# Kernel optimization log

Hardware: AMD Instinct MI355X
Metric: run time of the kernel (lower is better)

Reference implementation:

```python
import jax, jax.numpy as jnp
import numpy as np

EPS = 1e-5
SLOPE = 0.2

def _leaky(x):
    return jnp.where(x >= 0, x, SLOPE * x)

def _bn(x, g, b, axes):
    # batch-norm in training mode: biased stats over `axes`, per remaining channel dim
    mu = jnp.mean(x, axis=axes, keepdims=True)
    var = jnp.var(x, axis=axes, keepdims=True)
    shape = [1] * x.ndim
    shape[2 if x.ndim == 5 else 1] = -1
    return (x - mu) * jax.lax.rsqrt(var + EPS) * g.reshape(shape) + b.reshape(shape)

def setup_inputs() -> dict:
    key = jax.random.key(0)
    ks = jax.random.split(key, 6)
    T, B, C, H, W, D = 17, 16, 512, 16, 16, 256
    return {
        "cond": jax.random.normal(ks[0], (B, D), jnp.float32),
        "xbar": jax.random.normal(ks[1], (T, B, C, H, W), jnp.float32),
        "lin_w": jax.random.normal(ks[2], (D, D), jnp.float32) * 0.05,
        "lin_b": jnp.zeros((D,), jnp.float32),
        "bn_s_g": jnp.ones((D,), jnp.float32),
        "bn_s_b": jnp.zeros((D,), jnp.float32),
        "conv1_w": jax.random.normal(ks[3], (C, C), jnp.float32) * 0.05,
        "bn1_g": jnp.ones((C,), jnp.float32),
        "bn1_b": jnp.zeros((C,), jnp.float32),
        "conv2_w": jax.random.normal(ks[4], (C, C + D), jnp.float32) * 0.05,
        "bn2_g": jnp.ones((C,), jnp.float32),
        "bn2_b": jnp.zeros((C,), jnp.float32),
        "conv3_w": jax.random.normal(ks[5], (1, C, 2, 2), jnp.float32) * 0.05,
    }

def reference(cond, xbar, lin_w, lin_b, bn_s_g, bn_s_b, conv1_w, bn1_g, bn1_b, conv2_w, bn2_g, bn2_b, conv3_w):
    # sent_map: Linear -> BatchNorm1d (over batch) -> LeakyReLU
    sent = cond @ lin_w.T + lin_b                       # [B, D]
    sent = _leaky(_bn(sent, bn_s_g, bn_s_b, axes=(0,)))

    motions = xbar[1:] - xbar[:-1]                      # [F, B, C, H, W]
    F, B, C, H, W = motions.shape

    # motion_map: 1x1 conv -> BN (per-frame stats, matching the python loop) -> LeakyReLU
    h = jnp.einsum('fbchw,oc->fbohw', motions, conv1_w)
    h = _leaky(_bn(h, bn1_g, bn1_b, axes=(1, 3, 4)))

    # broadcast sentence vector over space (replaces per-pixel python loop)
    sent_dupe = jnp.broadcast_to(sent[None, :, :, None, None], (F, B, sent.shape[1], H, W))
    ms = jnp.concatenate([h, sent_dupe], axis=2)        # [F, B, C+D, H, W]

    # predictor: 1x1 conv -> BN (per-frame) -> LeakyReLU -> 2x2 stride-2 conv
    h2 = jnp.einsum('fbchw,oc->fbohw', ms, conv2_w)
    h2 = _leaky(_bn(h2, bn2_g, bn2_b, axes=(1, 3, 4)))

    h2f = h2.reshape(F * B, C, H, W)
    out = jax.lax.conv_general_dilated(
        h2f, conv3_w, window_strides=(2, 2), padding='VALID',
        dimension_numbers=('NCHW', 'OIHW', 'NCHW'))     # [F*B, 1, H/2, W/2]
    return out.reshape(F, B, -1)                        # matches view(B,-1) per frame + stack
```

## Files before the change

### kernel.cpp

```cpp
#include <hip/hip_runtime.h>
#include <hip/hip_bf16.h>

#define EPS 1e-5f
#define SLOPE 0.2f

#define NF 16
#define NBATCH 16
#define NC 512
#define NHW 256
#define ND 256
#define K2 768
#define MF 4096
#define FRAME_ELEMS ((size_t)MF * NC)

typedef __attribute__((ext_vector_type(8))) short short8;
typedef __attribute__((ext_vector_type(4))) float float4v;

__device__ __forceinline__ float lrelu(float v) { return v >= 0.f ? v : SLOPE * v; }
__device__ __forceinline__ float b2f(ushort u) { union { float f; uint i; } x; x.i = ((uint)u) << 16; return x.f; }
__device__ __forceinline__ ushort f2b(float f) {
  uint i = __float_as_uint(f);
  return (ushort)((i + 0x7FFFu + ((i >> 16) & 1u)) >> 16);
}
__device__ __forceinline__ void gl16(const ushort* g, ushort* l) {
  __builtin_amdgcn_global_load_lds(
      (const __attribute__((address_space(1))) unsigned int*)g,
      (__attribute__((address_space(3))) unsigned int*)l, 16, 0, 0);
}

__global__ __launch_bounds__(256) void k_pre(
    const float* __restrict__ w1, const float* __restrict__ w2,
    const float* __restrict__ cond, const float* __restrict__ lin_w,
    const float* __restrict__ lin_b, const float* __restrict__ gam,
    const float* __restrict__ bet,
    ushort* __restrict__ w1b, ushort* __restrict__ w2b,
    float* __restrict__ sent) {
  int bx = blockIdx.x, t = threadIdx.x;
  if (bx < 1024) {
    int i = bx * 256 + t;
    w1b[i] = f2b(w1[i]);
    int o = i >> 9, c = i & 511;
    w2b[i] = f2b(w2[(size_t)o * K2 + c]);
    return;
  }
  int d = t;
  float acc[NBATCH];
  float bias = lin_b[d];
#pragma unroll
  for (int b = 0; b < NBATCH; ++b) acc[b] = bias;
  for (int k = 0; k < ND; ++k) {
    float w = lin_w[d * ND + k];
#pragma unroll
    for (int b = 0; b < NBATCH; ++b) acc[b] = fmaf(cond[b * ND + k], w, acc[b]);
  }
  float mu = 0.f;
#pragma unroll
  for (int b = 0; b < NBATCH; ++b) mu += acc[b];
  mu *= (1.f / NBATCH);
  float var = 0.f;
#pragma unroll
  for (int b = 0; b < NBATCH; ++b) { float x = acc[b] - mu; var = fmaf(x, x, var); }
  var *= (1.f / NBATCH);
  float sc = rsqrtf(var + EPS) * gam[d];
  float sh = bet[d] - mu * sc;
#pragma unroll
  for (int b = 0; b < NBATCH; ++b) sent[b * ND + d] = lrelu(fmaf(acc[b], sc, sh));
}

__global__ __launch_bounds__(256) void k_mot(
    const float* __restrict__ xbar, ushort* __restrict__ mot, int f0, int nb,
    const float* __restrict__ sent, const float* __restrict__ w2,
    float* __restrict__ bias2) {
  int t = threadIdx.x;
  if (blockIdx.x == 32) {
    if (blockIdx.z != 0 || blockIdx.y >= 2) return;
    int o = blockIdx.y * 256 + t;
    float acc[NBATCH];
#pragma unroll
    for (int b = 0; b < NBATCH; ++b) acc[b] = 0.f;
    for (int d = 0; d < ND; ++d) {
      float w = w2[(size_t)o * K2 + NC + d];
#pragma unroll
      for (int b = 0; b < NBATCH; ++b) acc[b] = fmaf(sent[b * ND + d], w, acc[b]);
    }
#pragma unroll
    for (int b = 0; b < NBATCH; ++b) bias2[b * NC + o] = acc[b];
    return;
  }

  __shared__ float T[64][65];
  int b = blockIdx.y;
  int hw0 = (blockIdx.x & 3) * 64;
  int c0 = (blockIdx.x >> 2) * 64;
  int w = t >> 6, l = t & 63;
  int fr = blockIdx.z;

  const float* x0 = xbar + ((size_t)(f0 + fr) * NBATCH + b) * (NC * NHW) + hw0 + l;
  const float* x1 = x0 + (size_t)NBATCH * NC * NHW;
  float d[16];
#pragma unroll
  for (int k = 0; k < 16; ++k) {
    size_t off = (size_t)(c0 + 4 * k + w) * NHW;
    d[k] = x1[off] - x0[off];
  }
#pragma unroll
  for (int k = 0; k < 16; ++k) T[4 * k + w][l] = d[k];
  __syncthreads();
  ushort* mp = mot + ((size_t)fr * MF + b * NHW + hw0) * NC + c0;
#pragma unroll
  for (int k = 0; k < 16; ++k) mp[(size_t)(4 * k + w) * NC + l] = f2b(T[l][4 * k + w]);
}

template <int BIAS>
__global__ __launch_bounds__(512, 2) void k_gemm8(
    const ushort* __restrict__ A, const ushort* __restrict__ W,
    const float* __restrict__ bias2, ushort* __restrict__ H,
    float2* __restrict__ part) {
  __shared__ ushort lds[65536];
  const int t = threadIdx.x, w = t >> 6, l = t & 63;
  const int g = blockIdx.z, bx = blockIdx.x, ny = blockIdx.y;
  const int m0 = bx * 256, n0 = ny * 256;
  const int wr = w >> 2, wc = w & 3;

  const ushort* Ag = A + (size_t)g * FRAME_ELEMS + (size_t)m0 * NC;
  const ushort* Wg = W + (size_t)n0 * NC;

  size_t goff[4];
  int loff[4];
#pragma unroll
  for (int q = 0; q < 4; ++q) {
    int u = w * 256 + q * 64 + l;
    int row = u >> 3, cb = (u & 7) ^ (row & 7);
    goff[q] = (size_t)row * NC + cb * 8;
    loff[q] = u * 8;
  }

#define STAGE8(t_, b_)                                               \
  do {                                                               \
    const int k0_ = (t_) * 64;                                       \
    _Pragma("unroll") for (int q = 0; q < 4; ++q)                    \
        gl16(Ag + goff[q] + k0_, &lds[(b_) * 32768 + loff[q]]);      \
    _Pragma("unroll") for (int q = 0; q < 4; ++q)                    \
        gl16(Wg + goff[q] + k0_, &lds[(b_) * 32768 + 16384 + loff[q]]); \
  } while (0)

  int slot[2];
#pragma unroll
  for (int kk = 0; kk < 2; ++kk) slot[kk] = (((kk * 4 + (l >> 4)) ^ (l & 7)) * 8);

  float4v acc[8][4];
#pragma unroll
  for (int i = 0; i < 8; ++i)
#pragma unroll
    for (int j = 0; j < 4; ++j) acc[i][j] = (float4v)0.f;

  STAGE8(0, 0);
  STAGE8(1, 1);
  asm volatile("s_waitcnt vmcnt(8)" ::: "memory");
  __builtin_amdgcn_sched_barrier(0);
  __builtin_amdgcn_s_barrier();
  __builtin_amdgcn_sched_barrier(0);

#pragma unroll
  for (int kt = 0; kt < 8; ++kt) {
    const int b = kt & 1;
    const ushort* la = &lds[b * 32768];
    const ushort* lb = la + 16384;
    short8 bf[4][2], af[4][2];
#pragma unroll
    for (int fn = 0; fn < 4; ++fn) {
      int r = wc * 64 + fn * 16 + (l & 15);
#pragma unroll
      for (int kk = 0; kk < 2; ++kk)
        bf[fn][kk] = *(const short8*)&lb[r * 64 + slot[kk]];
    }
#pragma unroll
    for (int fm = 0; fm < 4; ++fm) {
      int r = wr * 128 + fm * 16 + (l & 15);
#pragma unroll
      for (int kk = 0; kk < 2; ++kk)
        af[fm][kk] = *(const short8*)&la[r * 64 + slot[kk]];
    }
    asm volatile("s_waitcnt lgkmcnt(0)" ::: "memory");
    __builtin_amdgcn_sched_barrier(0);
    __builtin_amdgcn_s_setprio(1);
#pragma unroll
    for (int kk = 0; kk < 2; ++kk)
#pragma unroll
      for (int fm = 0; fm < 4; ++fm)
#pragma unroll
        for (int fn = 0; fn < 4; ++fn)
          acc[fm][fn] = __builtin_amdgcn_mfma_f32_16x16x32_bf16(
              af[fm][kk], bf[fn][kk], acc[fm][fn], 0, 0, 0);
    __builtin_amdgcn_s_setprio(0);
#pragma unroll
    for (int fm = 0; fm < 4; ++fm) {
      int r = wr * 128 + 64 + fm * 16 + (l & 15);
#pragma unroll
      for (int kk = 0; kk < 2; ++kk)
        af[fm][kk] = *(const short8*)&la[r * 64 + slot[kk]];
    }
    asm volatile("s_waitcnt lgkmcnt(0)" ::: "memory");
    __builtin_amdgcn_sched_barrier(0);
    __builtin_amdgcn_s_barrier();
    __builtin_amdgcn_sched_barrier(0);
    if (kt < 6) STAGE8(kt + 2, b);
    __builtin_amdgcn_s_setprio(1);
#pragma unroll
    for (int kk = 0; kk < 2; ++kk)
#pragma unroll
      for (int fm = 0; fm < 4; ++fm)
#pragma unroll
        for (int fn = 0; fn < 4; ++fn)
          acc[fm + 4][fn] = __builtin_amdgcn_mfma_f32_16x16x32_bf16(
              af[fm][kk], bf[fn][kk], acc[fm + 4][fn], 0, 0, 0);
    __builtin_amdgcn_s_setprio(0);
    if (kt < 7) {
      if (kt < 6) asm volatile("s_waitcnt vmcnt(8)" ::: "memory");
      else        asm volatile("s_waitcnt vmcnt(0)" ::: "memory");
      __builtin_amdgcn_sched_barrier(0);
      __builtin_amdgcn_s_barrier();
      __builtin_amdgcn_sched_barrier(0);
    }
  }
#undef STAGE8

  __builtin_amdgcn_sched_barrier(0);
  __builtin_amdgcn_s_barrier();
  __builtin_amdgcn_sched_barrier(0);

  float bz[4];
#pragma unroll
  for (int fn = 0; fn < 4; ++fn)
    bz[fn] = BIAS ? bias2[bx * NC + n0 + wc * 64 + fn * 16 + (l & 15)] : 0.f;

  float sv[4], qv[4];
#pragma unroll
  for (int fn = 0; fn < 4; ++fn) {
    float s = 0.f, q = 0.f;
#pragma unroll
    for (int fm = 0; fm < 8; ++fm)
#pragma unroll
      for (int j = 0; j < 4; ++j) {
        float v = acc[fm][fn][j] + bz[fn];
        acc[fm][fn][j] = v;
        s += v;
        q = fmaf(v, v, q);
      }
    s += __shfl_xor(s, 16); s += __shfl_xor(s, 32);
    q += __shfl_xor(q, 16); q += __shfl_xor(q, 32);
    sv[fn] = s; qv[fn] = q;
  }
  if (l < 16) {
    int mb = bx * 2 + wr;
    float2* pp = part + ((size_t)g * 32 + mb) * NC + n0 + wc * 64 + l;
#pragma unroll
    for (int fn = 0; fn < 4; ++fn) pp[fn * 16] = make_float2(sv[fn], qv[fn]);
  }

  ushort* ep = &lds[w * 1088];
  ushort* Hg = H + ((size_t)g * MF + m0 + wr * 128) * NC + n0 + wc * 64;
#pragma unroll
  for (int fm = 0; fm < 8; ++fm) {
#pragma unroll
    for (int fn = 0; fn < 4; ++fn)
#pragma unroll
      for (int j = 0; j < 4; ++j)
        ep[((l >> 4) * 4 + j) * 68 + fn * 16 + (l & 15)] = f2b(acc[fm][fn][j]);
#pragma unroll
    for (int h = 0; h < 2; ++h) {
      int r = h * 8 + (l >> 3), sl = l & 7;
      short8 v = *(const short8*)&ep[r * 68 + sl * 8];
      *(short8*)&Hg[(size_t)(fm * 16 + r) * NC + sl * 8] = v;
    }
  }
}

__global__ __launch_bounds__(256) void k_stats2(
    const float2* __restrict__ part, const float* __restrict__ gam,
    const float* __restrict__ bet, float2* __restrict__ st) {
  int bi = blockIdx.x;
  int g = bi >> 1;
  int o = (bi & 1) * 256 + threadIdx.x;
  float s = 0.f, q = 0.f;
#pragma unroll
  for (int mb = 0; mb < 32; ++mb) {
    float2 v = part[((size_t)g * 32 + mb) * NC + o];
    s += v.x;
    q += v.y;
  }
  float mu = s * (1.f / 4096.f);
  float var = q * (1.f / 4096.f) - mu * mu;
  float sc = rsqrtf(var + EPS) * gam[o];
  st[g * NC + o] = make_float2(sc, bet[o] - mu * sc);
}

__global__ __launch_bounds__(256) void k_act(
    const ushort* __restrict__ h1, const float2* __restrict__ st,
    ushort* __restrict__ a1) {
  int g = blockIdx.z;
  size_t i0 = ((size_t)blockIdx.x * 256 + threadIdx.x) * 8;
  int o0 = (int)(i0 & 511);
  const ushort* src = h1 + (size_t)g * FRAME_ELEMS + i0;
  ushort* dst = a1 + (size_t)g * FRAME_ELEMS + i0;
  short8 v = *(const short8*)src;
  short8 r;
#pragma unroll
  for (int e = 0; e < 8; ++e) {
    float2 ss = st[g * NC + o0 + e];
    float x = fmaf(b2f((ushort)v[e]), ss.x, ss.y);
    r[e] = (short)f2b(lrelu(x));
  }
  *(short8*)dst = r;
}

__global__ __launch_bounds__(256) void k_conv3(
    const ushort* __restrict__ h2, const float2* __restrict__ st2,
    const float* __restrict__ w3, float* __restrict__ out, int f0) {
  int g = blockIdx.z;
  int b = blockIdx.x >> 2;
  int q = blockIdx.x & 3;
  int t = threadIdx.x;
  int oi = q * 16 + (t >> 4);
  int cs = t & 15;
  int y = oi >> 3, x = oi & 7;
  const ushort* base = h2 + ((size_t)g * MF + b * NHW) * NC;
  int m00 = (2 * y) * 16 + 2 * x;
  float acc = 0.f;
#pragma unroll
  for (int c8 = cs * 32; c8 < cs * 32 + 32; c8 += 8) {
    short8 v0 = *(const short8*)&base[(size_t)(m00 + 0) * NC + c8];
    short8 v1 = *(const short8*)&base[(size_t)(m00 + 1) * NC + c8];
    short8 v2 = *(const short8*)&base[(size_t)(m00 + 16) * NC + c8];
    short8 v3 = *(const short8*)&base[(size_t)(m00 + 17) * NC + c8];
#pragma unroll
    for (int e = 0; e < 8; ++e) {
      float2 ss = st2[g * NC + c8 + e];
      float4 wv = ((const float4*)w3)[c8 + e];
      acc = fmaf(lrelu(fmaf(b2f((ushort)v0[e]), ss.x, ss.y)), wv.x, acc);
      acc = fmaf(lrelu(fmaf(b2f((ushort)v1[e]), ss.x, ss.y)), wv.y, acc);
      acc = fmaf(lrelu(fmaf(b2f((ushort)v2[e]), ss.x, ss.y)), wv.z, acc);
      acc = fmaf(lrelu(fmaf(b2f((ushort)v3[e]), ss.x, ss.y)), wv.w, acc);
    }
  }
  acc += __shfl_xor(acc, 1);
  acc += __shfl_xor(acc, 2);
  acc += __shfl_xor(acc, 4);
  acc += __shfl_xor(acc, 8);
  if (cs == 0) out[((size_t)(f0 + g) * NBATCH + b) * 64 + oi] = acc;
}

extern "C" void kernel_launch(void* const* d_in, const int* in_sizes, int n_in,
                              void* d_out, int out_size, void* d_ws, size_t ws_size,
                              hipStream_t stream) {
  const float* cond = (const float*)d_in[0];
  const float* xbar = (const float*)d_in[1];
  const float* lin_w = (const float*)d_in[2];
  const float* lin_b = (const float*)d_in[3];
  const float* bnsg = (const float*)d_in[4];
  const float* bnsb = (const float*)d_in[5];
  const float* w1 = (const float*)d_in[6];
  const float* bn1g = (const float*)d_in[7];
  const float* bn1b = (const float*)d_in[8];
  const float* w2 = (const float*)d_in[9];
  const float* bn2g = (const float*)d_in[10];
  const float* bn2b = (const float*)d_in[11];
  const float* w3 = (const float*)d_in[12];
  float* out = (float*)d_out;

  char* p = (char*)d_ws;
  float* sent = (float*)p;    p += ((NBATCH * ND * 4 + 255) & ~255);
  float* bias2 = (float*)p;   p += ((NBATCH * NC * 4 + 255) & ~255);
  float2* st1 = (float2*)p;   p += ((NF * NC * 8 + 255) & ~255);
  float2* st2 = (float2*)p;   p += ((NF * NC * 8 + 255) & ~255);
  float2* part = (float2*)p;  p += (((size_t)NF * 32 * NC * 8 + 255) & ~255);
  ushort* w1b = (ushort*)p;   p += ((NC * NC * 2 + 255) & ~255);
  ushort* w2b = (ushort*)p;   p += ((NC * NC * 2 + 255) & ~255);
  size_t used = (size_t)(p - (char*)d_ws);
  const size_t frame_bytes = FRAME_ELEMS * 2;
  size_t rem = ws_size > used ? ws_size - used : 0;
  int FB = (int)(rem / (3 * frame_bytes));
  if (FB < 1) FB = 1;
  if (FB > NF) FB = NF;
  ushort* bufA = (ushort*)p;
  ushort* bufB = bufA + (size_t)FB * FRAME_ELEMS;
  ushort* bufC = bufB + (size_t)FB * FRAME_ELEMS;

  k_pre<<<1025, 256, 0, stream>>>(w1, w2, cond, lin_w, lin_b, bnsg, bnsb,
                                  w1b, w2b, sent);

  for (int f0 = 0; f0 < NF; f0 += FB) {
    int nb = (NF - f0) < FB ? (NF - f0) : FB;
    k_mot<<<dim3(33, NBATCH, nb), 256, 0, stream>>>(xbar, bufA, f0, nb,
                                                    sent, w2, bias2);
    k_gemm8<0><<<dim3(16, 2, nb), 512, 0, stream>>>(bufA, w1b, nullptr, bufB, part);
    k_stats2<<<2 * nb, 256, 0, stream>>>(part, bn1g, bn1b, st1);
    k_act<<<dim3(1024, 1, nb), 256, 0, stream>>>(bufB, st1, bufA);
    k_gemm8<1><<<dim3(16, 2, nb), 512, 0, stream>>>(bufA, w2b, bias2, bufC, part);
    k_stats2<<<2 * nb, 256, 0, stream>>>(part, bn2g, bn2b, st2);
    k_conv3<<<dim3(NBATCH * 4, 1, nb), 256, 0, stream>>>(bufC, st2, w3, out, f0);
  }
}
```

Measured before the change: 262.6 us.

## Fuse motion diff into GEMM1 loader and BN1 activation into GEMM2 loader

The first GEMM now reads xbar directly, computes the frame difference, converts to bf16 and transposes into LDS inside the main loop, replacing the separate k_mot kernel. The second GEMM applies BN1 scale/shift and LeakyReLU while staging its A operand, removing the k_act kernel and one full intermediate buffer round trip. The sentence bias computation moves into k_pre. This cuts HBM traffic and launches, but puts register-path loads, conversions and vmcnt(0) waits into the GEMM pipelines, which can stall MFMA issue. The first GEMM also reads fp32 xbar (twice the bytes of the old bf16 operand) through uncoalesced-to-LDS register paths.

```diff
diff --git a/kernel.cpp b/kernel.cpp
--- a/kernel.cpp
+++ b/kernel.cpp
@@ -27,6 +27,7 @@
       (const __attribute__((address_space(1))) unsigned int*)g,
       (__attribute__((address_space(3))) unsigned int*)l, 16, 0, 0);
 }
+#define SB __builtin_amdgcn_sched_barrier(0)
 
 __global__ __launch_bounds__(256) void k_pre(
     const float* __restrict__ w1, const float* __restrict__ w2,
@@ -34,7 +35,7 @@
     const float* __restrict__ lin_b, const float* __restrict__ gam,
     const float* __restrict__ bet,
     ushort* __restrict__ w1b, ushort* __restrict__ w2b,
-    float* __restrict__ sent) {
+    float* __restrict__ bias2) {
   int bx = blockIdx.x, t = threadIdx.x;
   if (bx < 1024) {
     int i = bx * 256 + t;
@@ -43,197 +44,54 @@
     w2b[i] = f2b(w2[(size_t)o * K2 + c]);
     return;
   }
+  __shared__ float sl[NBATCH][ND];
   int d = t;
-  float acc[NBATCH];
-  float bias = lin_b[d];
-#pragma unroll
-  for (int b = 0; b < NBATCH; ++b) acc[b] = bias;
-  for (int k = 0; k < ND; ++k) {
-    float w = lin_w[d * ND + k];
-#pragma unroll
-    for (int b = 0; b < NBATCH; ++b) acc[b] = fmaf(cond[b * ND + k], w, acc[b]);
-  }
-  float mu = 0.f;
-#pragma unroll
-  for (int b = 0; b < NBATCH; ++b) mu += acc[b];
-  mu *= (1.f / NBATCH);
-  float var = 0.f;
-#pragma unroll
-  for (int b = 0; b < NBATCH; ++b) { float x = acc[b] - mu; var = fmaf(x, x, var); }
-  var *= (1.f / NBATCH);
-  float sc = rsqrtf(var + EPS) * gam[d];
-  float sh = bet[d] - mu * sc;
-#pragma unroll
-  for (int b = 0; b < NBATCH; ++b) sent[b * ND + d] = lrelu(fmaf(acc[b], sc, sh));
-}
-
-__global__ __launch_bounds__(256) void k_mot(
-    const float* __restrict__ xbar, ushort* __restrict__ mot, int f0, int nb,
-    const float* __restrict__ sent, const float* __restrict__ w2,
-    float* __restrict__ bias2) {
-  int t = threadIdx.x;
-  if (blockIdx.x == 32) {
-    if (blockIdx.z != 0 || blockIdx.y >= 2) return;
-    int o = blockIdx.y * 256 + t;
+  {
     float acc[NBATCH];
-#pragma unroll
-    for (int b = 0; b < NBATCH; ++b) acc[b] = 0.f;
-    for (int d = 0; d < ND; ++d) {
-      float w = w2[(size_t)o * K2 + NC + d];
-#pragma unroll
-      for (int b = 0; b < NBATCH; ++b) acc[b] = fmaf(sent[b * ND + d], w, acc[b]);
-    }
-#pragma unroll
-    for (int b = 0; b < NBATCH; ++b) bias2[b * NC + o] = acc[b];
-    return;
-  }
-
-  __shared__ float T[64][65];
-  int b = blockIdx.y;
-  int hw0 = (blockIdx.x & 3) * 64;
-  int c0 = (blockIdx.x >> 2) * 64;
-  int w = t >> 6, l = t & 63;
-  int fr = blockIdx.z;
-
-  const float* x0 = xbar + ((size_t)(f0 + fr) * NBATCH + b) * (NC * NHW) + hw0 + l;
-  const float* x1 = x0 + (size_t)NBATCH * NC * NHW;
-  float d[16];
-#pragma unroll
-  for (int k = 0; k < 16; ++k) {
-    size_t off = (size_t)(c0 + 4 * k + w) * NHW;
-    d[k] = x1[off] - x0[off];
-  }
-#pragma unroll
-  for (int k = 0; k < 16; ++k) T[4 * k + w][l] = d[k];
+    float bias = lin_b[d];
+#pragma unroll
+    for (int b = 0; b < NBATCH; ++b) acc[b] = bias;
+    for (int k = 0; k < ND; ++k) {
+      float w = lin_w[d * ND + k];
+#pragma unroll
+      for (int b = 0; b < NBATCH; ++b) acc[b] = fmaf(cond[b * ND + k], w, acc[b]);
+    }
+    float mu = 0.f;
+#pragma unroll
+    for (int b = 0; b < NBATCH; ++b) mu += acc[b];
+    mu *= (1.f / NBATCH);
+    float var = 0.f;
+#pragma unroll
+    for (int b = 0; b < NBATCH; ++b) { float x = acc[b] - mu; var = fmaf(x, x, var); }
+    var *= (1.f / NBATCH);
+    float sc = rsqrtf(var + EPS) * gam[d];
+    float sh = bet[d] - mu * sc;
+#pragma unroll
+    for (int b = 0; b < NBATCH; ++b) sl[b][d] = lrelu(fmaf(acc[b], sc, sh));
+  }
   __syncthreads();
-  ushort* mp = mot + ((size_t)fr * MF + b * NHW + hw0) * NC + c0;
-#pragma unroll
-  for (int k = 0; k < 16; ++k) mp[(size_t)(4 * k + w) * NC + l] = f2b(T[l][4 * k + w]);
-}
-
-template <int BIAS>
-__global__ __launch_bounds__(512, 2) void k_gemm8(
-    const ushort* __restrict__ A, const ushort* __restrict__ W,
-    const float* __restrict__ bias2, ushort* __restrict__ H,
-    float2* __restrict__ part) {
-  __shared__ ushort lds[65536];
-  const int t = threadIdx.x, w = t >> 6, l = t & 63;
-  const int g = blockIdx.z, bx = blockIdx.x, ny = blockIdx.y;
-  const int m0 = bx * 256, n0 = ny * 256;
-  const int wr = w >> 2, wc = w & 3;
-
-  const ushort* Ag = A + (size_t)g * FRAME_ELEMS + (size_t)m0 * NC;
-  const ushort* Wg = W + (size_t)n0 * NC;
-
-  size_t goff[4];
-  int loff[4];
-#pragma unroll
-  for (int q = 0; q < 4; ++q) {
-    int u = w * 256 + q * 64 + l;
-    int row = u >> 3, cb = (u & 7) ^ (row & 7);
-    goff[q] = (size_t)row * NC + cb * 8;
-    loff[q] = u * 8;
-  }
-
-#define STAGE8(t_, b_)                                               \
-  do {                                                               \
-    const int k0_ = (t_) * 64;                                       \
-    _Pragma("unroll") for (int q = 0; q < 4; ++q)                    \
-        gl16(Ag + goff[q] + k0_, &lds[(b_) * 32768 + loff[q]]);      \
-    _Pragma("unroll") for (int q = 0; q < 4; ++q)                    \
-        gl16(Wg + goff[q] + k0_, &lds[(b_) * 32768 + 16384 + loff[q]]); \
-  } while (0)
-
-  int slot[2];
-#pragma unroll
-  for (int kk = 0; kk < 2; ++kk) slot[kk] = (((kk * 4 + (l >> 4)) ^ (l & 7)) * 8);
-
-  float4v acc[8][4];
-#pragma unroll
-  for (int i = 0; i < 8; ++i)
-#pragma unroll
-    for (int j = 0; j < 4; ++j) acc[i][j] = (float4v)0.f;
-
-  STAGE8(0, 0);
-  STAGE8(1, 1);
-  asm volatile("s_waitcnt vmcnt(8)" ::: "memory");
-  __builtin_amdgcn_sched_barrier(0);
-  __builtin_amdgcn_s_barrier();
-  __builtin_amdgcn_sched_barrier(0);
-
-#pragma unroll
-  for (int kt = 0; kt < 8; ++kt) {
-    const int b = kt & 1;
-    const ushort* la = &lds[b * 32768];
-    const ushort* lb = la + 16384;
-    short8 bf[4][2], af[4][2];
-#pragma unroll
-    for (int fn = 0; fn < 4; ++fn) {
-      int r = wc * 64 + fn * 16 + (l & 15);
-#pragma unroll
-      for (int kk = 0; kk < 2; ++kk)
-        bf[fn][kk] = *(const short8*)&lb[r * 64 + slot[kk]];
-    }
-#pragma unroll
-    for (int fm = 0; fm < 4; ++fm) {
-      int r = wr * 128 + fm * 16 + (l & 15);
-#pragma unroll
-      for (int kk = 0; kk < 2; ++kk)
-        af[fm][kk] = *(const short8*)&la[r * 64 + slot[kk]];
-    }
-    asm volatile("s_waitcnt lgkmcnt(0)" ::: "memory");
-    __builtin_amdgcn_sched_barrier(0);
-    __builtin_amdgcn_s_setprio(1);
-#pragma unroll
-    for (int kk = 0; kk < 2; ++kk)
-#pragma unroll
-      for (int fm = 0; fm < 4; ++fm)
-#pragma unroll
-        for (int fn = 0; fn < 4; ++fn)
-          acc[fm][fn] = __builtin_amdgcn_mfma_f32_16x16x32_bf16(
-              af[fm][kk], bf[fn][kk], acc[fm][fn], 0, 0, 0);
-    __builtin_amdgcn_s_setprio(0);
-#pragma unroll
-    for (int fm = 0; fm < 4; ++fm) {
-      int r = wr * 128 + 64 + fm * 16 + (l & 15);
-#pragma unroll
-      for (int kk = 0; kk < 2; ++kk)
-        af[fm][kk] = *(const short8*)&la[r * 64 + slot[kk]];
-    }
-    asm volatile("s_waitcnt lgkmcnt(0)" ::: "memory");
-    __builtin_amdgcn_sched_barrier(0);
-    __builtin_amdgcn_s_barrier();
-    __builtin_amdgcn_sched_barrier(0);
-    if (kt < 6) STAGE8(kt + 2, b);
-    __builtin_amdgcn_s_setprio(1);
-#pragma unroll
-    for (int kk = 0; kk < 2; ++kk)
-#pragma unroll
-      for (int fm = 0; fm < 4; ++fm)
-#pragma unroll
-        for (int fn = 0; fn < 4; ++fn)
-          acc[fm + 4][fn] = __builtin_amdgcn_mfma_f32_16x16x32_bf16(
-              af[fm][kk], bf[fn][kk], acc[fm + 4][fn], 0, 0, 0);
-    __builtin_amdgcn_s_setprio(0);
-    if (kt < 7) {
-      if (kt < 6) asm volatile("s_waitcnt vmcnt(8)" ::: "memory");
-      else        asm volatile("s_waitcnt vmcnt(0)" ::: "memory");
-      __builtin_amdgcn_sched_barrier(0);
-      __builtin_amdgcn_s_barrier();
-      __builtin_amdgcn_sched_barrier(0);
-    }
-  }
-#undef STAGE8
-
-  __builtin_amdgcn_sched_barrier(0);
-  __builtin_amdgcn_s_barrier();
-  __builtin_amdgcn_sched_barrier(0);
-
+  int o = (bx - 1024) * 256 + t;
+  float acc2[NBATCH];
+#pragma unroll
+  for (int b = 0; b < NBATCH; ++b) acc2[b] = 0.f;
+  for (int d2 = 0; d2 < ND; ++d2) {
+    float wv = w2[(size_t)o * K2 + NC + d2];
+#pragma unroll
+    for (int b = 0; b < NBATCH; ++b) acc2[b] = fmaf(sl[b][d2], wv, acc2[b]);
+  }
+#pragma unroll
+  for (int b = 0; b < NBATCH; ++b) bias2[b * NC + o] = acc2[b];
+}
+
+__device__ __forceinline__ void gemm_epi(
+    float4v (&acc)[8][4], ushort* lds, const float* bias2, int has_bias,
+    ushort* __restrict__ H, float2* __restrict__ part,
+    int g, int bx, int n0, int w, int l, int wr, int wc) {
+  int m0 = bx * 256;
   float bz[4];
 #pragma unroll
   for (int fn = 0; fn < 4; ++fn)
-    bz[fn] = BIAS ? bias2[bx * NC + n0 + wc * 64 + fn * 16 + (l & 15)] : 0.f;
-
+    bz[fn] = has_bias ? bias2[bx * NC + n0 + wc * 64 + fn * 16 + (l & 15)] : 0.f;
   float sv[4], qv[4];
 #pragma unroll
   for (int fn = 0; fn < 4; ++fn) {
@@ -257,7 +115,6 @@
 #pragma unroll
     for (int fn = 0; fn < 4; ++fn) pp[fn * 16] = make_float2(sv[fn], qv[fn]);
   }
-
   ushort* ep = &lds[w * 1088];
   ushort* Hg = H + ((size_t)g * MF + m0 + wr * 128) * NC + n0 + wc * 64;
 #pragma unroll
@@ -274,6 +131,292 @@
       *(short8*)&Hg[(size_t)(fm * 16 + r) * NC + sl * 8] = v;
     }
   }
+}
+
+__global__ __launch_bounds__(512, 2) void k_gemm1f(
+    const float* __restrict__ xbar, const ushort* __restrict__ W,
+    ushort* __restrict__ H, float2* __restrict__ part, int f0) {
+  __shared__ ushort lds[65536];
+  const int t = threadIdx.x, w = t >> 6, l = t & 63;
+  const int g = blockIdx.z, bx = blockIdx.x, ny = blockIdx.y;
+  const int n0 = ny * 256;
+  const int wr = w >> 2, wc = w & 3;
+
+  const ushort* Wg = W + (size_t)n0 * NC;
+  size_t goff[4];
+  int loff[4];
+#pragma unroll
+  for (int q = 0; q < 4; ++q) {
+    int u = w * 256 + q * 64 + l;
+    int row = u >> 3, cb = (u & 7) ^ (row & 7);
+    goff[q] = (size_t)row * NC + cb * 8;
+    loff[q] = u * 8;
+  }
+  const float* x0 = xbar + (((size_t)(f0 + g) * NBATCH + bx) * NC + w * 8) * NHW + l * 4;
+  const float* x1 = x0 + (size_t)NBATCH * NC * NHW;
+
+  int slot[2];
+#pragma unroll
+  for (int kk = 0; kk < 2; ++kk) slot[kk] = (((kk * 4 + (l >> 4)) ^ (l & 7)) * 8);
+  const int swbase = w;
+
+  float4 p0[4], p1[4];
+#define AISSUE(h_, kt_)                                                      \
+  do {                                                                       \
+    _Pragma("unroll") for (int cc = 0; cc < 4; ++cc) {                       \
+      size_t off = (size_t)((kt_) * 64 + (h_) * 4 + cc) * NHW;               \
+      p1[cc] = *(const float4*)(x1 + off);                                   \
+      p0[cc] = *(const float4*)(x0 + off);                                   \
+    }                                                                        \
+  } while (0)
+#define ATRANS(h_, b_)                                                       \
+  do {                                                                       \
+    _Pragma("unroll") for (int i = 0; i < 4; ++i) {                          \
+      int hw = l * 4 + i;                                                    \
+      uint lo = (uint)f2b(((const float*)&p1[0])[i] - ((const float*)&p0[0])[i]) | \
+                ((uint)f2b(((const float*)&p1[1])[i] - ((const float*)&p0[1])[i]) << 16); \
+      uint hi = (uint)f2b(((const float*)&p1[2])[i] - ((const float*)&p0[2])[i]) | \
+                ((uint)f2b(((const float*)&p1[3])[i] - ((const float*)&p0[3])[i]) << 16); \
+      uint2 pk = make_uint2(lo, hi);                                         \
+      *(uint2*)&lds[(b_) * 32768 + hw * 64 + ((swbase ^ (hw & 7)) * 8) + (h_) * 4] = pk; \
+    }                                                                        \
+  } while (0)
+#define WSTAGE(t_, b_)                                                       \
+  do {                                                                       \
+    _Pragma("unroll") for (int q = 0; q < 4; ++q)                            \
+        gl16(Wg + goff[q] + (t_) * 64, &lds[(b_) * 32768 + 16384 + loff[q]]); \
+  } while (0)
+
+  AISSUE(0, 0);
+  WSTAGE(0, 0);
+  WSTAGE(1, 1);
+  asm volatile("s_waitcnt vmcnt(0)" ::: "memory"); SB;
+  ATRANS(0, 0);
+  AISSUE(1, 0);
+  asm volatile("s_waitcnt vmcnt(0)" ::: "memory"); SB;
+  ATRANS(1, 0);
+  asm volatile("s_waitcnt lgkmcnt(0)" ::: "memory"); SB;
+  __builtin_amdgcn_s_barrier(); SB;
+
+  float4v acc[8][4];
+#pragma unroll
+  for (int i = 0; i < 8; ++i)
+#pragma unroll
+    for (int j = 0; j < 4; ++j) acc[i][j] = (float4v)0.f;
+
+#pragma unroll
+  for (int kt = 0; kt < 8; ++kt) {
+    const int cur = kt & 1;
+    const ushort* la = &lds[cur * 32768];
+    const ushort* lb = la + 16384;
+    if (kt < 7) AISSUE(0, kt + 1);
+    short8 bf[4][2], af[4][2];
+#pragma unroll
+    for (int fn = 0; fn < 4; ++fn) {
+      int r = wc * 64 + fn * 16 + (l & 15);
+#pragma unroll
+      for (int kk = 0; kk < 2; ++kk) bf[fn][kk] = *(const short8*)&lb[r * 64 + slot[kk]];
+    }
+#pragma unroll
+    for (int fm = 0; fm < 4; ++fm) {
+      int r = wr * 128 + fm * 16 + (l & 15);
+#pragma unroll
+      for (int kk = 0; kk < 2; ++kk) af[fm][kk] = *(const short8*)&la[r * 64 + slot[kk]];
+    }
+    asm volatile("s_waitcnt lgkmcnt(0)" ::: "memory"); SB;
+    __builtin_amdgcn_s_setprio(1);
+#pragma unroll
+    for (int kk = 0; kk < 2; ++kk)
+#pragma unroll
+      for (int fm = 0; fm < 4; ++fm)
+#pragma unroll
+        for (int fn = 0; fn < 4; ++fn)
+          acc[fm][fn] = __builtin_amdgcn_mfma_f32_16x16x32_bf16(
+              af[fm][kk], bf[fn][kk], acc[fm][fn], 0, 0, 0);
+    __builtin_amdgcn_s_setprio(0);
+#pragma unroll
+    for (int fm = 0; fm < 4; ++fm) {
+      int r = wr * 128 + 64 + fm * 16 + (l & 15);
+#pragma unroll
+      for (int kk = 0; kk < 2; ++kk) af[fm][kk] = *(const short8*)&la[r * 64 + slot[kk]];
+    }
+    asm volatile("s_waitcnt lgkmcnt(0)" ::: "memory"); SB;
+    __builtin_amdgcn_s_barrier(); SB;
+    if (kt < 7) {
+      asm volatile("s_waitcnt vmcnt(0)" ::: "memory"); SB;
+      ATRANS(0, cur ^ 1);
+      AISSUE(1, kt + 1);
+      asm volatile("s_waitcnt vmcnt(0)" ::: "memory"); SB;
+      ATRANS(1, cur ^ 1);
+    }
+    if (kt < 6) WSTAGE(kt + 2, cur);
+    __builtin_amdgcn_s_setprio(1);
+#pragma unroll
+    for (int kk = 0; kk < 2; ++kk)
+#pragma unroll
+      for (int fm = 0; fm < 4; ++fm)
+#pragma unroll
+        for (int fn = 0; fn < 4; ++fn)
+          acc[fm + 4][fn] = __builtin_amdgcn_mfma_f32_16x16x32_bf16(
+              af[fm][kk], bf[fn][kk], acc[fm + 4][fn], 0, 0, 0);
+    __builtin_amdgcn_s_setprio(0);
+    if (kt < 7) {
+      asm volatile("s_waitcnt lgkmcnt(0)" ::: "memory"); SB;
+      __builtin_amdgcn_s_barrier(); SB;
+    }
+  }
+#undef AISSUE
+#undef ATRANS
+#undef WSTAGE
+  SB; __builtin_amdgcn_s_barrier(); SB;
+  gemm_epi(acc, lds, nullptr, 0, H, part, g, bx, n0, w, l, wr, wc);
+}
+
+__global__ __launch_bounds__(512, 2) void k_gemm2f(
+    const ushort* __restrict__ A, const ushort* __restrict__ W,
+    const float2* __restrict__ st, const float* __restrict__ bias2,
+    ushort* __restrict__ H, float2* __restrict__ part) {
+  __shared__ ushort lds[65536];
+  __shared__ float2 stl[NC];
+  const int t = threadIdx.x, w = t >> 6, l = t & 63;
+  const int g = blockIdx.z, bx = blockIdx.x, ny = blockIdx.y;
+  const int m0 = bx * 256, n0 = ny * 256;
+  const int wr = w >> 2, wc = w & 3;
+
+  const ushort* Wg = W + (size_t)n0 * NC;
+  const ushort* Ab = A + ((size_t)g * MF + m0) * NC;
+  size_t goff[4], agoff[4];
+  int loff[4], arow[4];
+#pragma unroll
+  for (int q = 0; q < 4; ++q) {
+    int u = w * 256 + q * 64 + l;
+    int row = u >> 3, cb = (u & 7) ^ (row & 7);
+    goff[q] = (size_t)row * NC + cb * 8;
+    loff[q] = u * 8;
+    arow[q] = row;
+    agoff[q] = (size_t)row * NC + (l & 7) * 8;
+  }
+  int slot[2];
+#pragma unroll
+  for (int kk = 0; kk < 2; ++kk) slot[kk] = (((kk * 4 + (l >> 4)) ^ (l & 7)) * 8);
+
+  short8 ar[4];
+  float2 sr[8];
+#define A2ISSUE(kt_)                                                         \
+  do {                                                                       \
+    _Pragma("unroll") for (int q = 0; q < 4; ++q)                            \
+        ar[q] = *(const short8*)(Ab + agoff[q] + (kt_) * 64);                \
+  } while (0)
+#define SRREAD(kt_)                                                          \
+  do {                                                                       \
+    _Pragma("unroll") for (int e = 0; e < 8; ++e)                            \
+        sr[e] = stl[(kt_) * 64 + (l & 7) * 8 + e];                           \
+  } while (0)
+#define A2TRANS(b_)                                                          \
+  do {                                                                       \
+    _Pragma("unroll") for (int q = 0; q < 4; ++q) {                          \
+      uint out[4];                                                           \
+      _Pragma("unroll") for (int j = 0; j < 4; ++j) {                        \
+        float xa = fmaf(b2f((ushort)ar[q][2 * j]), sr[2 * j].x, sr[2 * j].y); \
+        float xb = fmaf(b2f((ushort)ar[q][2 * j + 1]), sr[2 * j + 1].x, sr[2 * j + 1].y); \
+        xa = fmaxf(xa, SLOPE * xa);                                          \
+        xb = fmaxf(xb, SLOPE * xb);                                          \
+        out[j] = (uint)f2b(xa) | ((uint)f2b(xb) << 16);                      \
+      }                                                                      \
+      *(uint4*)&lds[(b_) * 32768 + arow[q] * 64 + (((l & 7) ^ (arow[q] & 7)) * 8)] = \
+          *(const uint4*)out;                                                \
+    }                                                                        \
+  } while (0)
+#define WSTAGE2(t_, b_)                                                      \
+  do {                                                                       \
+    _Pragma("unroll") for (int q = 0; q < 4; ++q)                            \
+        gl16(Wg + goff[q] + (t_) * 64, &lds[(b_) * 32768 + 16384 + loff[q]]); \
+  } while (0)
+
+  stl[t] = st[(size_t)g * NC + t];
+  if (t + 512 < NC) {}
+  A2ISSUE(0);
+  WSTAGE2(0, 0);
+  WSTAGE2(1, 1);
+  asm volatile("s_waitcnt lgkmcnt(0)" ::: "memory"); SB;
+  __builtin_amdgcn_s_barrier(); SB;
+  SRREAD(0);
+  asm volatile("s_waitcnt vmcnt(0) lgkmcnt(0)" ::: "memory"); SB;
+  A2TRANS(0);
+  asm volatile("s_waitcnt lgkmcnt(0)" ::: "memory"); SB;
+  __builtin_amdgcn_s_barrier(); SB;
+
+  float4v acc[8][4];
+#pragma unroll
+  for (int i = 0; i < 8; ++i)
+#pragma unroll
+    for (int j = 0; j < 4; ++j) acc[i][j] = (float4v)0.f;
+
+#pragma unroll
+  for (int kt = 0; kt < 8; ++kt) {
+    const int cur = kt & 1;
+    const ushort* la = &lds[cur * 32768];
+    const ushort* lb = la + 16384;
+    if (kt < 7) A2ISSUE(kt + 1);
+    short8 bf[4][2], af[4][2];
+#pragma unroll
+    for (int fn = 0; fn < 4; ++fn) {
+      int r = wc * 64 + fn * 16 + (l & 15);
+#pragma unroll
+      for (int kk = 0; kk < 2; ++kk) bf[fn][kk] = *(const short8*)&lb[r * 64 + slot[kk]];
+    }
+#pragma unroll
+    for (int fm = 0; fm < 4; ++fm) {
+      int r = wr * 128 + fm * 16 + (l & 15);
+#pragma unroll
+      for (int kk = 0; kk < 2; ++kk) af[fm][kk] = *(const short8*)&la[r * 64 + slot[kk]];
+    }
+    asm volatile("s_waitcnt lgkmcnt(0)" ::: "memory"); SB;
+    __builtin_amdgcn_s_setprio(1);
+#pragma unroll
+    for (int kk = 0; kk < 2; ++kk)
+#pragma unroll
+      for (int fm = 0; fm < 4; ++fm)
+#pragma unroll
+        for (int fn = 0; fn < 4; ++fn)
+          acc[fm][fn] = __builtin_amdgcn_mfma_f32_16x16x32_bf16(
+              af[fm][kk], bf[fn][kk], acc[fm][fn], 0, 0, 0);
+    __builtin_amdgcn_s_setprio(0);
+#pragma unroll
+    for (int fm = 0; fm < 4; ++fm) {
+      int r = wr * 128 + 64 + fm * 16 + (l & 15);
+#pragma unroll
+      for (int kk = 0; kk < 2; ++kk) af[fm][kk] = *(const short8*)&la[r * 64 + slot[kk]];
+    }
+    asm volatile("s_waitcnt lgkmcnt(0)" ::: "memory"); SB;
+    __builtin_amdgcn_s_barrier(); SB;
+    if (kt < 7) {
+      SRREAD(kt + 1);
+      asm volatile("s_waitcnt vmcnt(0) lgkmcnt(0)" ::: "memory"); SB;
+      A2TRANS(cur ^ 1);
+    }
+    if (kt < 6) WSTAGE2(kt + 2, cur);
+    __builtin_amdgcn_s_setprio(1);
+#pragma unroll
+    for (int kk = 0; kk < 2; ++kk)
+#pragma unroll
+      for (int fm = 0; fm < 4; ++fm)
+#pragma unroll
+        for (int fn = 0; fn < 4; ++fn)
+          acc[fm + 4][fn] = __builtin_amdgcn_mfma_f32_16x16x32_bf16(
+              af[fm][kk], bf[fn][kk], acc[fm + 4][fn], 0, 0, 0);
+    __builtin_amdgcn_s_setprio(0);
+    if (kt < 7) {
+      asm volatile("s_waitcnt lgkmcnt(0)" ::: "memory"); SB;
+      __builtin_amdgcn_s_barrier(); SB;
+    }
+  }
+#undef A2ISSUE
+#undef SRREAD
+#undef A2TRANS
+#undef WSTAGE2
+  SB; __builtin_amdgcn_s_barrier(); SB;
+  gemm_epi(acc, lds, bias2, 1, H, part, g, bx, n0, w, l, wr, wc);
 }
 
 __global__ __launch_bounds__(256) void k_stats2(
@@ -293,25 +436,6 @@
   float var = q * (1.f / 4096.f) - mu * mu;
   float sc = rsqrtf(var + EPS) * gam[o];
   st[g * NC + o] = make_float2(sc, bet[o] - mu * sc);
-}
-
-__global__ __launch_bounds__(256) void k_act(
-    const ushort* __restrict__ h1, const float2* __restrict__ st,
-    ushort* __restrict__ a1) {
-  int g = blockIdx.z;
-  size_t i0 = ((size_t)blockIdx.x * 256 + threadIdx.x) * 8;
-  int o0 = (int)(i0 & 511);
-  const ushort* src = h1 + (size_t)g * FRAME_ELEMS + i0;
-  ushort* dst = a1 + (size_t)g * FRAME_ELEMS + i0;
-  short8 v = *(const short8*)src;
-  short8 r;
-#pragma unroll
-  for (int e = 0; e < 8; ++e) {
-    float2 ss = st[g * NC + o0 + e];
-    float x = fmaf(b2f((ushort)v[e]), ss.x, ss.y);
-    r[e] = (short)f2b(lrelu(x));
-  }
-  *(short8*)dst = r;
 }
 
 __global__ __launch_bounds__(256) void k_conv3(
@@ -369,7 +493,6 @@
   float* out = (float*)d_out;
 
   char* p = (char*)d_ws;
-  float* sent = (float*)p;    p += ((NBATCH * ND * 4 + 255) & ~255);
   float* bias2 = (float*)p;   p += ((NBATCH * NC * 4 + 255) & ~255);
   float2* st1 = (float2*)p;   p += ((NF * NC * 8 + 255) & ~255);
   float2* st2 = (float2*)p;   p += ((NF * NC * 8 + 255) & ~255);
@@ -379,24 +502,20 @@
   size_t used = (size_t)(p - (char*)d_ws);
   const size_t frame_bytes = FRAME_ELEMS * 2;
   size_t rem = ws_size > used ? ws_size - used : 0;
-  int FB = (int)(rem / (3 * frame_bytes));
+  int FB = (int)(rem / (2 * frame_bytes));
   if (FB < 1) FB = 1;
   if (FB > NF) FB = NF;
-  ushort* bufA = (ushort*)p;
-  ushort* bufB = bufA + (size_t)FB * FRAME_ELEMS;
+  ushort* bufB = (ushort*)p;
   ushort* bufC = bufB + (size_t)FB * FRAME_ELEMS;
 
-  k_pre<<<1025, 256, 0, stream>>>(w1, w2, cond, lin_w, lin_b, bnsg, bnsb,
-                                  w1b, w2b, sent);
+  k_pre<<<1026, 256, 0, stream>>>(w1, w2, cond, lin_w, lin_b, bnsg, bnsb,
+                                  w1b, w2b, bias2);
 
   for (int f0 = 0; f0 < NF; f0 += FB) {
     int nb = (NF - f0) < FB ? (NF - f0) : FB;
-    k_mot<<<dim3(33, NBATCH, nb), 256, 0, stream>>>(xbar, bufA, f0, nb,
-                                                    sent, w2, bias2);
-    k_gemm8<0><<<dim3(16, 2, nb), 512, 0, stream>>>(bufA, w1b, nullptr, bufB, part);
+    k_gemm1f<<<dim3(16, 2, nb), 512, 0, stream>>>(xbar, w1b, bufB, part, f0);
     k_stats2<<<2 * nb, 256, 0, stream>>>(part, bn1g, bn1b, st1);
-    k_act<<<dim3(1024, 1, nb), 256, 0, stream>>>(bufB, st1, bufA);
-    k_gemm8<1><<<dim3(16, 2, nb), 512, 0, stream>>>(bufA, w2b, bias2, bufC, part);
+    k_gemm2f<<<dim3(16, 2, nb), 512, 0, stream>>>(bufB, w2b, st1, bias2, bufC, part);
     k_stats2<<<2 * nb, 256, 0, stream>>>(part, bn2g, bn2b, st2);
     k_conv3<<<dim3(NBATCH * 4, 1, nb), 256, 0, stream>>>(bufC, st2, w3, out, f0);
   }
```

New measurement: 313.6 us. 19.4% more time.
